# Kernel optimization log

Measured on AMD Instinct MI355X. Metric: run time of the kernel, lower is better.

## Reference

```python
import jax, jax.numpy as jnp
import numpy as np

NUM_CLASSES = 100
EPS = 1e-8  # torch F.cosine_similarity default eps


def setup_inputs() -> dict:
    key = jax.random.key(0)
    k1, k2 = jax.random.split(key)
    feat = jax.random.normal(k1, (100000, 512), dtype=jnp.float32)
    label = jax.random.randint(k2, (100000,), 0, NUM_CLASSES, dtype=jnp.int64)
    return {"feat": feat, "label": label}


def reference(feat, label):
    # Per-class mean (segment mean) -- replaces the Python loop over classes.
    sums = jax.ops.segment_sum(feat, label, num_segments=NUM_CLASSES)          # [C, D]
    counts = jax.ops.segment_sum(jnp.ones_like(label, dtype=feat.dtype), label,
                                 num_segments=NUM_CLASSES)                      # [C]
    means = sums / jnp.maximum(counts, 1.0)[:, None]                            # [C, D]

    # Only the gathered (own-class) column of the sim matrix is returned,
    # so compute cos(feat[i], means[label[i]]) directly.
    cent = means[label]                                                         # [N, D]
    dot = jnp.sum(feat * cent, axis=-1)                                         # [N]
    n_feat = jnp.maximum(jnp.linalg.norm(feat, axis=-1), EPS)
    n_cent = jnp.maximum(jnp.linalg.norm(cent, axis=-1), EPS)
    return dot / (n_feat * n_cent)
```

## Files before the change

### kernel.cpp

```cpp
#include <hip/hip_runtime.h>
#include <hip/hip_bf16.h>

#define NCLS 100
#define DIM  512
#define EPSV 1e-8f
#define NSPLIT 16
#define IDXBUF 512
#define SCAT_ROWS 1024

__global__ __launch_bounds__(256) void hist_kernel(const int* __restrict__ label,
                                                   int* __restrict__ cnt, int n) {
    __shared__ int h[NCLS];
    for (int i = threadIdx.x; i < NCLS; i += 256) h[i] = 0;
    __syncthreads();
    for (int i = blockIdx.x * 256 + threadIdx.x; i < n; i += gridDim.x * 256)
        atomicAdd(&h[label[i]], 1);
    __syncthreads();
    for (int i = threadIdx.x; i < NCLS; i += 256) {
        int v = h[i];
        if (v) atomicAdd(&cnt[i], v);
    }
}

__global__ void scan_kernel(const int* __restrict__ cnt, int* __restrict__ base,
                            int* __restrict__ cursor) {
    if (threadIdx.x == 0) {
        int s = 0;
        for (int c = 0; c < NCLS; ++c) { base[c] = s; cursor[c] = s; s += cnt[c]; }
    }
}

__global__ __launch_bounds__(256) void scatter_kernel(const int* __restrict__ label,
                                                      int* __restrict__ cursor,
                                                      int* __restrict__ perm, int n) {
    __shared__ int h[NCLS];
    __shared__ int starts[NCLS];
    const int tid = threadIdx.x;
    for (int i = tid; i < NCLS; i += 256) h[i] = 0;
    __syncthreads();

    const int r0 = blockIdx.x * SCAT_ROWS;
    int c[4], lr[4];
    #pragma unroll
    for (int k = 0; k < 4; ++k) {
        const int r = r0 + k * 256 + tid;
        if (r < n) { c[k] = label[r]; lr[k] = atomicAdd(&h[c[k]], 1); }
        else c[k] = -1;
    }
    __syncthreads();
    for (int i = tid; i < NCLS; i += 256)
        starts[i] = h[i] ? atomicAdd(&cursor[i], h[i]) : 0;
    __syncthreads();
    #pragma unroll
    for (int k = 0; k < 4; ++k)
        if (c[k] >= 0) perm[starts[c[k]] + lr[k]] = r0 + k * 256 + tid;
}

__global__ __launch_bounds__(256) void segsum_kernel(const float* __restrict__ feat,
                                                     const int* __restrict__ perm,
                                                     const int* __restrict__ base,
                                                     const int* __restrict__ cnt,
                                                     float* __restrict__ sums) {
    const int s = blockIdx.x;
    const int c = blockIdx.y;
    const int m = cnt[c];
    const int b = base[c];
    const int jlo = b + (m * s) / NSPLIT;
    const int jhi = b + (m * (s + 1)) / NSPLIT;

    __shared__ int idx[IDXBUF];
    const int tid = threadIdx.x;
    float2 acc = {0.0f, 0.0f};
    const float* fbase = feat + tid * 2;

    for (int j0 = jlo; j0 < jhi; j0 += IDXBUF) {
        const int batch = min(IDXBUF, jhi - j0);
        __syncthreads();
        for (int i = tid; i < batch; i += 256) idx[i] = perm[j0 + i];
        __syncthreads();
        int i = 0;
        for (; i + 8 <= batch; i += 8) {
            float2 v[8];
            #pragma unroll
            for (int u = 0; u < 8; ++u)
                v[u] = *(const float2*)(fbase + (size_t)idx[i + u] * DIM);
            #pragma unroll
            for (int u = 0; u < 8; ++u) { acc.x += v[u].x; acc.y += v[u].y; }
        }
        for (; i < batch; ++i) {
            float2 v = *(const float2*)(fbase + (size_t)idx[i] * DIM);
            acc.x += v.x; acc.y += v.y;
        }
    }
    if (jhi > jlo) {
        atomicAdd(&sums[(size_t)c * DIM + tid * 2],     acc.x);
        atomicAdd(&sums[(size_t)c * DIM + tid * 2 + 1], acc.y);
    }
}

__global__ __launch_bounds__(256) void finalize_kernel(const float* __restrict__ sums,
                                                       const int* __restrict__ cnt,
                                                       float* __restrict__ means,
                                                       float* __restrict__ qinv) {
    const int c = blockIdx.x;
    const float inv = 1.0f / fmaxf((float)cnt[c], 1.0f);
    __shared__ float red[4];
    float ss = 0.0f;
    for (int d = threadIdx.x; d < DIM; d += 256) {
        float m = sums[(size_t)c * DIM + d] * inv;
        means[(size_t)c * DIM + d] = m;
        ss += m * m;
    }
    #pragma unroll
    for (int off = 32; off; off >>= 1) ss += __shfl_down(ss, off, 64);
    const int wv = threadIdx.x >> 6, ln = threadIdx.x & 63;
    if (ln == 0) red[wv] = ss;
    __syncthreads();
    if (threadIdx.x == 0) {
        float t = red[0] + red[1] + red[2] + red[3];
        qinv[c] = 1.0f / fmaxf(sqrtf(t), EPSV);
    }
}

__global__ __launch_bounds__(256) void cos_kernel(const float* __restrict__ feat,
                                                  const int* __restrict__ label,
                                                  const float* __restrict__ means,
                                                  const float* __restrict__ qinv,
                                                  float* __restrict__ out, int n) {
    const int lane = threadIdx.x & 63;
    const int wv   = threadIdx.x >> 6;
    const int cl   = lane >> 4;
    const int t    = lane & 15;

    const int row = blockIdx.x * 16 + wv * 4 + cl;
    const bool ok = row < n;
    const int rr = ok ? row : (n - 1);

    const int c = label[rr];
    const float4* f4 = (const float4*)(feat  + (size_t)rr * DIM);
    const float4* m4 = (const float4*)(means + (size_t)c  * DIM);

    float4 a[8], b[8];
    #pragma unroll
    for (int j = 0; j < 8; ++j) a[j] = f4[t + 16 * j];
    #pragma unroll
    for (int j = 0; j < 8; ++j) b[j] = m4[t + 16 * j];

    float dot = 0.0f, nf = 0.0f;
    #pragma unroll
    for (int j = 0; j < 8; ++j) {
        dot += a[j].x * b[j].x + a[j].y * b[j].y + a[j].z * b[j].z + a[j].w * b[j].w;
        nf  += a[j].x * a[j].x + a[j].y * a[j].y + a[j].z * a[j].z + a[j].w * a[j].w;
    }

    #pragma unroll
    for (int off = 8; off; off >>= 1) {
        dot += __shfl_xor(dot, off, 64);
        nf  += __shfl_xor(nf,  off, 64);
    }
    if (t == 0 && ok) {
        float nfv = fmaxf(sqrtf(nf), EPSV);
        out[row] = dot * qinv[c] / nfv;
    }
}

extern "C" void kernel_launch(void* const* d_in, const int* in_sizes, int n_in,
                              void* d_out, int out_size, void* d_ws, size_t ws_size,
                              hipStream_t stream) {
    const float* feat  = (const float*)d_in[0];
    const int*   label = (const int*)d_in[1];
    float*       out   = (float*)d_out;
    const int n = in_sizes[0] / DIM;

    float* sums   = (float*)d_ws;
    int*   cnt    = (int*)(sums + NCLS * DIM);
    float* means  = (float*)(cnt + 128);
    float* qinv   = means + NCLS * DIM;
    int*   base   = (int*)(qinv + 128);
    int*   cursor = base + 128;
    int*   perm   = cursor + 128;

    hipMemsetAsync(d_ws, 0, (NCLS * DIM + 128) * sizeof(float), stream);

    hist_kernel<<<160, 256, 0, stream>>>(label, cnt, n);
    scan_kernel<<<1, 64, 0, stream>>>(cnt, base, cursor);
    scatter_kernel<<<(n + SCAT_ROWS - 1) / SCAT_ROWS, 256, 0, stream>>>(label, cursor, perm, n);

    dim3 sg(NSPLIT, NCLS);
    segsum_kernel<<<sg, 256, 0, stream>>>(feat, perm, base, cnt, sums);

    finalize_kernel<<<NCLS, 256, 0, stream>>>(sums, cnt, means, qinv);

    cos_kernel<<<(n + 15) / 16, 256, 0, stream>>>(feat, label, means, qinv, out, n);
}
```

Before: 334.3 us.

## Parallelize class scan, widen segsum loads to float4, prenormalize class means

The single-thread serial scan becomes a 128-thread shared-memory Hillis-Steele prefix sum. The segment-sum kernel now has each half-block take alternating rows with float4 loads, so each thread issues wider gathers, at the cost of four atomics per thread. The finalize kernel stores unit-normalized means, which removes the qinv lookup and multiply from the cosine kernel. The cosine output now divides the dot product with the normalized mean by the feature norm.

After: 332.5 us (median of 2 runs). Within noise of the previous version (-0.6%).

```diff
diff --git a/kernel.cpp b/kernel.cpp
--- a/kernel.cpp
+++ b/kernel.cpp
@@ -22,11 +22,24 @@
     }
 }
 
-__global__ void scan_kernel(const int* __restrict__ cnt, int* __restrict__ base,
-                            int* __restrict__ cursor) {
-    if (threadIdx.x == 0) {
-        int s = 0;
-        for (int c = 0; c < NCLS; ++c) { base[c] = s; cursor[c] = s; s += cnt[c]; }
+__global__ __launch_bounds__(128) void scan_kernel(const int* __restrict__ cnt,
+                                                   int* __restrict__ base,
+                                                   int* __restrict__ cursor) {
+    __shared__ int a[128];
+    const int t = threadIdx.x;
+    a[t] = (t < NCLS) ? cnt[t] : 0;
+    __syncthreads();
+    #pragma unroll
+    for (int off = 1; off < 128; off <<= 1) {
+        int v = (t >= off) ? a[t - off] : 0;
+        __syncthreads();
+        a[t] += v;
+        __syncthreads();
+    }
+    if (t < NCLS) {
+        int excl = a[t] - cnt[t];
+        base[t] = excl;
+        cursor[t] = excl;
     }
 }
 
@@ -69,63 +82,63 @@
     const int jhi = b + (m * (s + 1)) / NSPLIT;
 
     __shared__ int idx[IDXBUF];
-    const int tid = threadIdx.x;
-    float2 acc = {0.0f, 0.0f};
-    const float* fbase = feat + tid * 2;
+    const int tid  = threadIdx.x;
+    const int half = tid >> 7;
+    const int dq   = (tid & 127) * 4;
+
+    float4 acc = {0.0f, 0.0f, 0.0f, 0.0f};
 
     for (int j0 = jlo; j0 < jhi; j0 += IDXBUF) {
         const int batch = min(IDXBUF, jhi - j0);
         __syncthreads();
         for (int i = tid; i < batch; i += 256) idx[i] = perm[j0 + i];
         __syncthreads();
-        int i = 0;
-        for (; i + 8 <= batch; i += 8) {
-            float2 v[8];
+        int i = half;
+        for (; i + 14 < batch; i += 16) {
+            float4 v[8];
             #pragma unroll
             for (int u = 0; u < 8; ++u)
-                v[u] = *(const float2*)(fbase + (size_t)idx[i + u] * DIM);
+                v[u] = *(const float4*)(feat + (size_t)idx[i + 2 * u] * DIM + dq);
             #pragma unroll
-            for (int u = 0; u < 8; ++u) { acc.x += v[u].x; acc.y += v[u].y; }
+            for (int u = 0; u < 8; ++u) {
+                acc.x += v[u].x; acc.y += v[u].y; acc.z += v[u].z; acc.w += v[u].w;
+            }
         }
-        for (; i < batch; ++i) {
-            float2 v = *(const float2*)(fbase + (size_t)idx[i] * DIM);
-            acc.x += v.x; acc.y += v.y;
+        for (; i < batch; i += 2) {
+            float4 v = *(const float4*)(feat + (size_t)idx[i] * DIM + dq);
+            acc.x += v.x; acc.y += v.y; acc.z += v.z; acc.w += v.w;
         }
     }
-    if (jhi > jlo) {
-        atomicAdd(&sums[(size_t)c * DIM + tid * 2],     acc.x);
-        atomicAdd(&sums[(size_t)c * DIM + tid * 2 + 1], acc.y);
+    if (m > 0) {
+        float* dst = &sums[(size_t)c * DIM + dq];
+        atomicAdd(dst + 0, acc.x); atomicAdd(dst + 1, acc.y);
+        atomicAdd(dst + 2, acc.z); atomicAdd(dst + 3, acc.w);
     }
 }
 
 __global__ __launch_bounds__(256) void finalize_kernel(const float* __restrict__ sums,
                                                        const int* __restrict__ cnt,
-                                                       float* __restrict__ means,
-                                                       float* __restrict__ qinv) {
+                                                       float* __restrict__ mhat) {
     const int c = blockIdx.x;
     const float inv = 1.0f / fmaxf((float)cnt[c], 1.0f);
+    const int t = threadIdx.x;
+    float m0 = sums[(size_t)c * DIM + t] * inv;
+    float m1 = sums[(size_t)c * DIM + 256 + t] * inv;
+    float ss = m0 * m0 + m1 * m1;
+    #pragma unroll
+    for (int off = 32; off; off >>= 1) ss += __shfl_down(ss, off, 64);
     __shared__ float red[4];
-    float ss = 0.0f;
-    for (int d = threadIdx.x; d < DIM; d += 256) {
-        float m = sums[(size_t)c * DIM + d] * inv;
-        means[(size_t)c * DIM + d] = m;
-        ss += m * m;
-    }
-    #pragma unroll
-    for (int off = 32; off; off >>= 1) ss += __shfl_down(ss, off, 64);
-    const int wv = threadIdx.x >> 6, ln = threadIdx.x & 63;
-    if (ln == 0) red[wv] = ss;
-    __syncthreads();
-    if (threadIdx.x == 0) {
-        float t = red[0] + red[1] + red[2] + red[3];
-        qinv[c] = 1.0f / fmaxf(sqrtf(t), EPSV);
-    }
+    if ((t & 63) == 0) red[t >> 6] = ss;
+    __syncthreads();
+    const float tot = red[0] + red[1] + red[2] + red[3];
+    const float q = 1.0f / fmaxf(sqrtf(tot), EPSV);
+    mhat[(size_t)c * DIM + t] = m0 * q;
+    mhat[(size_t)c * DIM + 256 + t] = m1 * q;
 }
 
 __global__ __launch_bounds__(256) void cos_kernel(const float* __restrict__ feat,
                                                   const int* __restrict__ label,
-                                                  const float* __restrict__ means,
-                                                  const float* __restrict__ qinv,
+                                                  const float* __restrict__ mhat,
                                                   float* __restrict__ out, int n) {
     const int lane = threadIdx.x & 63;
     const int wv   = threadIdx.x >> 6;
@@ -137,8 +150,8 @@
     const int rr = ok ? row : (n - 1);
 
     const int c = label[rr];
-    const float4* f4 = (const float4*)(feat  + (size_t)rr * DIM);
-    const float4* m4 = (const float4*)(means + (size_t)c  * DIM);
+    const float4* f4 = (const float4*)(feat + (size_t)rr * DIM);
+    const float4* m4 = (const float4*)(mhat + (size_t)c  * DIM);
 
     float4 a[8], b[8];
     #pragma unroll
@@ -159,8 +172,7 @@
         nf  += __shfl_xor(nf,  off, 64);
     }
     if (t == 0 && ok) {
-        float nfv = fmaxf(sqrtf(nf), EPSV);
-        out[row] = dot * qinv[c] / nfv;
+        out[row] = dot / fmaxf(sqrtf(nf), EPSV);
     }
 }
 
@@ -174,22 +186,21 @@
 
     float* sums   = (float*)d_ws;
     int*   cnt    = (int*)(sums + NCLS * DIM);
-    float* means  = (float*)(cnt + 128);
-    float* qinv   = means + NCLS * DIM;
-    int*   base   = (int*)(qinv + 128);
+    float* mhat   = (float*)(cnt + 128);
+    int*   base   = (int*)(mhat + NCLS * DIM);
     int*   cursor = base + 128;
     int*   perm   = cursor + 128;
 
     hipMemsetAsync(d_ws, 0, (NCLS * DIM + 128) * sizeof(float), stream);
 
     hist_kernel<<<160, 256, 0, stream>>>(label, cnt, n);
-    scan_kernel<<<1, 64, 0, stream>>>(cnt, base, cursor);
+    scan_kernel<<<1, 128, 0, stream>>>(cnt, base, cursor);
     scatter_kernel<<<(n + SCAT_ROWS - 1) / SCAT_ROWS, 256, 0, stream>>>(label, cursor, perm, n);
 
     dim3 sg(NSPLIT, NCLS);
     segsum_kernel<<<sg, 256, 0, stream>>>(feat, perm, base, cnt, sums);
 
-    finalize_kernel<<<NCLS, 256, 0, stream>>>(sums, cnt, means, qinv);
-
-    cos_kernel<<<(n + 15) / 16, 256, 0, stream>>>(feat, label, means, qinv, out, n);
-}
+    finalize_kernel<<<NCLS, 256, 0, stream>>>(sums, cnt, mhat);
+
+    cos_kernel<<<(n + 15) / 16, 256, 0, stream>>>(feat, label, mhat, out, n);
+}
```
